# Optimization experiments

Measured on AMD Instinct MI355X. Metric: run time of the kernel, lower is better.

The kernel has to match this reference:

```python
import jax, jax.numpy as jnp
import numpy as np

N, E, IN, K, F, D = 50000, 800000, 256, 4, 64, 2


def setup_inputs() -> dict:
    key = jax.random.key(0)
    ks = jax.random.split(key, 10)
    # CSR rowptr: 0 .. E, nondecreasing, endpoints pinned
    inner = jnp.sort(jax.random.randint(ks[0], (N - 1,), 0, E + 1))
    rowptr = jnp.concatenate([jnp.zeros(1, jnp.int64), inner.astype(jnp.int64), jnp.full(1, E, jnp.int64)])
    colind = jax.random.randint(ks[1], (E,), 0, N).astype(jnp.int64)
    # CSC mirrors (used only by the fused kernel's backward; inert in forward math)
    inner_c = jnp.sort(jax.random.randint(ks[2], (N - 1,), 0, E + 1))
    colptr = jnp.concatenate([jnp.zeros(1, jnp.int64), inner_c.astype(jnp.int64), jnp.full(1, E, jnp.int64)])
    rowind = jax.random.randint(ks[3], (E,), 0, N).astype(jnp.int64)
    permute = jnp.arange(E, dtype=jnp.int64)
    feat = jax.random.normal(ks[4], (N, IN), dtype=jnp.float32)
    pseudo = jax.random.uniform(ks[5], (E, D), dtype=jnp.float32)
    # params: fc weight [K*F, IN] (xavier-normal style scale), mu ~ N(0, 0.1), inv_sigma = 1, bias = 0
    gain = float(np.sqrt(2.0))
    std = gain * float(np.sqrt(2.0 / (IN + K * F)))
    W_fc = jax.random.normal(ks[6], (K * F, IN), dtype=jnp.float32) * std
    mu = jax.random.normal(ks[7], (K, D), dtype=jnp.float32) * 0.1
    inv_sigma = jnp.ones((K, D), dtype=jnp.float32)
    bias = jnp.zeros((F,), dtype=jnp.float32)
    return {"rowptr": rowptr, "colind": colind, "colptr": colptr, "rowind": rowind,
            "permute": permute, "feat": feat, "pseudo": pseudo,
            "W_fc": W_fc, "mu": mu, "inv_sigma": inv_sigma, "bias": bias}


def reference(rowptr, colind, colptr, rowind, permute, feat, pseudo, W_fc, mu, inv_sigma, bias):
    n = feat.shape[0]
    e = colind.shape[0]
    k, d = mu.shape
    f = W_fc.shape[0] // k
    # dense projection: [N, K, F]
    node_feat = (feat @ W_fc.T).reshape(n, k, f)
    # per-edge Gaussian mixture weights: [E, K]
    diff = pseudo[:, None, :] - mu[None, :, :]              # [E, K, D]
    gaussian = jnp.exp(jnp.sum(-0.5 * diff * diff * (inv_sigma[None, :, :] ** 2), axis=-1))
    # multi-head SpMM: gather source feats, weight per kernel, sum kernels (sum commutes
    # with the segment reduction, so fold the head-sum into the edge message): [E, F]
    msg = jnp.einsum('ek,ekf->ef', gaussian, node_feat[colind])
    # destination node of each CSR edge
    dst = jnp.searchsorted(rowptr, jnp.arange(e), side='right') - 1
    rst = jax.ops.segment_sum(msg, dst, num_segments=n)      # [N, F]
    return rst + bias
```

## Files before the change

kernel.cpp:

```cpp
#include <hip/hip_runtime.h>


typedef _Float16 f16;
typedef __attribute__((ext_vector_type(4))) _Float16 f16x4;
typedef __attribute__((ext_vector_type(8))) _Float16 f16x8;
typedef __attribute__((ext_vector_type(4))) float f32x4;

__device__ inline f16x4 cvt4h(float4 v) {
    f16x4 h;
    h.x = (f16)v.x; h.y = (f16)v.y; h.z = (f16)v.z; h.w = (f16)v.w;
    return h;
}

__device__ inline int dot4_i8(int a, int b) {
#if __has_builtin(__builtin_amdgcn_sdot4)
    return __builtin_amdgcn_sdot4(a, b, 0, false);
#else
    return (int)(char)(a)       * (int)(char)(b)
         + (int)(char)(a >> 8)  * (int)(char)(b >> 8)
         + (int)(char)(a >> 16) * (int)(char)(b >> 16)
         + (int)(char)(a >> 24) * (int)(char)(b >> 24);
#endif
}

__global__ __launch_bounds__(256) void convert_W(
    const float* __restrict__ W, f16* __restrict__ Wp)
{
    const int gid = blockIdx.x * 256 + threadIdx.x;
    const int jp = gid >> 6, k4 = gid & 63;
    const int wrow = ((jp >> 4) & 3) * 64 + ((jp >> 6) << 4) + (jp & 15);
    const int k4s = k4 ^ ((jp & 3) << 1);
    reinterpret_cast<f16x4*>(Wp)[jp * 64 + k4s] =
        cvt4h(reinterpret_cast<const float4*>(W)[wrow * 64 + k4]);
}

__global__ __launch_bounds__(256) void gemm_fused(
    const float* __restrict__ feat,
    const f16* __restrict__ Wp,
    char* __restrict__ nfq,
    float* __restrict__ sc,
    int M)
{
    __shared__ char smem[32768 + 16384];
    char* Asb = smem;
    char* Bsb = smem + 32768;
    const int t    = threadIdx.x;
    const int lane = t & 63;
    const int wave = t >> 6;
    const int bm   = blockIdx.x * 64;
    const int l16  = lane & 15;
    const int quad = lane >> 4;
    const int wn   = wave * 64;

    size_t bsrc[4];
#pragma unroll
    for (int j = 0; j < 4; ++j)
        bsrc[j] = (size_t)(wave * 64 + j * 16 + (lane >> 2)) * 256 + (lane & 3) * 8;

    typedef __attribute__((address_space(3))) void lds_t;
    typedef const __attribute__((address_space(1))) void gm_t;

#pragma unroll
    for (int j = 0; j < 4; ++j)
        __builtin_amdgcn_global_load_lds((gm_t*)(Wp + bsrc[j]),
            (lds_t*)(Bsb + (wave * 4 + j) * 1024), 16, 0, 0);

#pragma unroll
    for (int it = 0; it < 8; ++it) {
        const int flat = it * 2048 + t * 8;
        const int row  = flat >> 8;
        const int koff = flat & 255;
        const float* src = feat + (size_t)min(bm + row, M - 1) * 256 + koff;
        const float4 a0 = *reinterpret_cast<const float4*>(src);
        const float4 a1 = *reinterpret_cast<const float4*>(src + 4);
        char* dst = Asb + row * 512 + ((koff * 2) ^ ((row & 7) << 4));
        *reinterpret_cast<f16x4*>(dst)     = cvt4h(a0);
        *reinterpret_cast<f16x4*>(dst + 8) = cvt4h(a1);
    }

    f32x4 acc[4][4];
#pragma unroll
    for (int mi = 0; mi < 4; ++mi)
#pragma unroll
        for (int ni = 0; ni < 4; ++ni)
            acc[mi][ni] = (f32x4){0.f, 0.f, 0.f, 0.f};

    __syncthreads();

    const int axor = (l16 & 7) << 4;
    const int bxor = (l16 & 3) << 4;

#pragma unroll
    for (int ki = 0; ki < 8; ++ki) {
        __builtin_amdgcn_sched_barrier(0);
        asm volatile("s_waitcnt vmcnt(0)" ::: "memory");
        __builtin_amdgcn_sched_barrier(0);

        f16x8 af[4], bfr[4];
#pragma unroll
        for (int mi = 0; mi < 4; ++mi)
            af[mi] = *reinterpret_cast<const f16x8*>(
                Asb + (mi * 16 + l16) * 512 + ((ki * 64 + quad * 16) ^ axor));
#pragma unroll
        for (int ni = 0; ni < 4; ++ni)
            bfr[ni] = *reinterpret_cast<const f16x8*>(
                Bsb + (wn + ni * 16 + l16) * 64 + ((quad << 4) ^ bxor));

        __builtin_amdgcn_sched_barrier(0);
        asm volatile("s_waitcnt lgkmcnt(0)" ::: "memory");
        __builtin_amdgcn_sched_barrier(0);

        if (ki < 7) {
            const int k0 = (ki + 1) * 32;
#pragma unroll
            for (int j = 0; j < 4; ++j)
                __builtin_amdgcn_global_load_lds((gm_t*)(Wp + bsrc[j] + k0),
                    (lds_t*)(Bsb + (wave * 4 + j) * 1024), 16, 0, 0);
        }

#pragma unroll
        for (int mi = 0; mi < 4; ++mi)
#pragma unroll
            for (int ni = 0; ni < 4; ++ni)
                acc[mi][ni] = __builtin_amdgcn_mfma_f32_16x16x32_f16(
                    af[mi], bfr[ni], acc[mi][ni], 0, 0, 0);
    }

#pragma unroll
    for (int mi = 0; mi < 4; ++mi) {
#pragma unroll
        for (int r = 0; r < 4; ++r) {
            float am = 0.f;
#pragma unroll
            for (int ni = 0; ni < 4; ++ni)
                am = fmaxf(am, fabsf(acc[mi][ni][r]));
            am = fmaxf(am, __shfl_xor(am, 1));
            am = fmaxf(am, __shfl_xor(am, 2));
            am = fmaxf(am, __shfl_xor(am, 4));
            am = fmaxf(am, __shfl_xor(am, 8));
            const float sinv = am > 0.f ? 127.f / am : 0.f;
            unsigned pk = 0;
#pragma unroll
            for (int k = 0; k < 4; ++k) {
                const int b = (int)__builtin_rintf(acc[mi][k][r] * sinv);
                pk |= (unsigned)(b & 255) << (8 * k);
            }
            const int rl  = mi * 16 + quad * 4 + r;
            const int row = bm + rl;
            if (row < M) {
                reinterpret_cast<unsigned*>(nfq + (size_t)row * 256)
                    [wave * 16 + l16] = pk;
                if (l16 == 0) sc[row * 4 + wave] = am * (1.f / 16129.f);
            }
        }
    }
}

__global__ __launch_bounds__(256) void edge_aggregate(
    const int* __restrict__ rowptr,
    const int* __restrict__ colind,
    const float* __restrict__ pseudo,
    const char* __restrict__ nfq,
    const float* __restrict__ sc,
    const float* __restrict__ mu,
    const float* __restrict__ inv_sigma,
    const float* __restrict__ bias,
    float* __restrict__ out,
    int N)
{
    const int lane = threadIdx.x & 63;
    const int wid  = blockIdx.x * 4 + (threadIdx.x >> 6);
    const int na   = wid * 2;
    if (na >= N) return;
    const int nb   = na + 1;
    const bool hb  = nb < N;

    const int fo   = lane & 15;
    const int eg   = lane >> 4;
    const int qoff = fo << 4;
    const int goff = fo >> 2;

    const int kk = lane >> 4;
    const float mx = mu[2 * kk], my = mu[2 * kk + 1];
    const float sa = inv_sigma[2 * kk], sb = inv_sigma[2 * kk + 1];
    const float C  = -0.5f * 1.4426950408889634f;
    const float cx = C * sa * sa, cy = C * sb * sb;
    const int   sh = kk * 8;

    auto gpack = [&](int ec, int e0, int e1) -> int {
        const int exm = ec + fo;
        const bool gv = exm < e1;
        const int safe = (e1 > e0) ? (e1 - 1) : 0;
        const int ex  = gv ? exm : safe;
        const float2 p = *reinterpret_cast<const float2*>(pseudo + 2 * (size_t)ex);
        const float dx = p.x - mx, dy = p.y - my;
        const float g = exp2f(fmaf(dy * dy, cy, dx * dx * cx));
        int b = gv ? (((int)(g * 127.f + 0.5f)) << sh) : 0;
        b |= __shfl_xor(b, 16);
        b |= __shfl_xor(b, 32);
        return b;
    };

    const int ea0 = rowptr[na];
    const int ea1 = rowptr[na + 1];
    const int eb0 = ea1;
    const int eb1 = hb ? rowptr[nb + 1] : ea1;

    const int safea = (ea1 > ea0) ? (ea1 - 1) : 0;
    int cfo_a = colind[min(ea0 + fo, safea)];
    int cfo_b = 0, gpk_b = 0;
    if (hb) {
        const int safeb = (eb1 > eb0) ? (eb1 - 1) : 0;
        cfo_b = colind[min(eb0 + fo, safeb)];
        gpk_b = gpack(eb0, eb0, eb1);
    }
    int gpk_a = gpack(ea0, ea0, ea1);

    float a0 = 0.f, a1 = 0.f, a2 = 0.f, a3 = 0.f;
    {
        int gpk = gpk_a, cfo = cfo_a;
        for (int ec = ea0; ec < ea1; ec += 16) {
            int4  q[4];
            float s[4];
            int   gq[4];
#pragma unroll
            for (int gi = 0; gi < 4; ++gi) {
                const int c = __shfl(cfo, gi * 4 + eg);
                q[gi]  = *reinterpret_cast<const int4*>(
                             nfq + ((size_t)c << 8) + qoff);
                s[gi]  = sc[c * 4 + goff];
                gq[gi] = __shfl(gpk, gi * 4 + eg);
            }
            const int ecn = ec + 16;
            int gpk_n = 0, cfo_n = cfo;
            if (ecn < ea1) {
                cfo_n = colind[min(ecn + fo, ea1 - 1)];
                gpk_n = gpack(ecn, ea0, ea1);
            }
#pragma unroll
            for (int gi = 0; gi < 4; ++gi) {
                a0 = fmaf(s[gi], (float)dot4_i8(q[gi].x, gq[gi]), a0);
                a1 = fmaf(s[gi], (float)dot4_i8(q[gi].y, gq[gi]), a1);
                a2 = fmaf(s[gi], (float)dot4_i8(q[gi].z, gq[gi]), a2);
                a3 = fmaf(s[gi], (float)dot4_i8(q[gi].w, gq[gi]), a3);
            }
            gpk = gpk_n; cfo = cfo_n;
        }
    }
    a0 += __shfl_xor(a0, 16); a0 += __shfl_xor(a0, 32);
    a1 += __shfl_xor(a1, 16); a1 += __shfl_xor(a1, 32);
    a2 += __shfl_xor(a2, 16); a2 += __shfl_xor(a2, 32);
    a3 += __shfl_xor(a3, 16); a3 += __shfl_xor(a3, 32);
    if (lane < 16) {
        const float4 b4 = reinterpret_cast<const float4*>(bias)[fo];
        float4 o;
        o.x = a0 + b4.x; o.y = a1 + b4.y; o.z = a2 + b4.z; o.w = a3 + b4.w;
        reinterpret_cast<float4*>(out + ((size_t)na << 6))[fo] = o;
    }

    if (!hb) return;
    float b0 = 0.f, b1 = 0.f, b2 = 0.f, b3 = 0.f;
    {
        int gpk = gpk_b, cfo = cfo_b;
        for (int ec = eb0; ec < eb1; ec += 16) {
            int4  q[4];
            float s[4];
            int   gq[4];
#pragma unroll
            for (int gi = 0; gi < 4; ++gi) {
                const int c = __shfl(cfo, gi * 4 + eg);
                q[gi]  = *reinterpret_cast<const int4*>(
                             nfq + ((size_t)c << 8) + qoff);
                s[gi]  = sc[c * 4 + goff];
                gq[gi] = __shfl(gpk, gi * 4 + eg);
            }
            const int ecn = ec + 16;
            int gpk_n = 0, cfo_n = cfo;
            if (ecn < eb1) {
                cfo_n = colind[min(ecn + fo, eb1 - 1)];
                gpk_n = gpack(ecn, eb0, eb1);
            }
#pragma unroll
            for (int gi = 0; gi < 4; ++gi) {
                b0 = fmaf(s[gi], (float)dot4_i8(q[gi].x, gq[gi]), b0);
                b1 = fmaf(s[gi], (float)dot4_i8(q[gi].y, gq[gi]), b1);
                b2 = fmaf(s[gi], (float)dot4_i8(q[gi].z, gq[gi]), b2);
                b3 = fmaf(s[gi], (float)dot4_i8(q[gi].w, gq[gi]), b3);
            }
            gpk = gpk_n; cfo = cfo_n;
        }
    }
    b0 += __shfl_xor(b0, 16); b0 += __shfl_xor(b0, 32);
    b1 += __shfl_xor(b1, 16); b1 += __shfl_xor(b1, 32);
    b2 += __shfl_xor(b2, 16); b2 += __shfl_xor(b2, 32);
    b3 += __shfl_xor(b3, 16); b3 += __shfl_xor(b3, 32);
    if (lane < 16) {
        const float4 b4 = reinterpret_cast<const float4*>(bias)[fo];
        float4 o;
        o.x = b0 + b4.x; o.y = b1 + b4.y; o.z = b2 + b4.z; o.w = b3 + b4.w;
        reinterpret_cast<float4*>(out + ((size_t)nb << 6))[fo] = o;
    }
}

extern "C" void kernel_launch(void* const* d_in, const int* in_sizes, int n_in,
                              void* d_out, int out_size, void* d_ws, size_t ws_size,
                              hipStream_t stream)
{
    const int*   rowptr    = (const int*)d_in[0];
    const int*   colind    = (const int*)d_in[1];
    const float* feat      = (const float*)d_in[5];
    const float* pseudo    = (const float*)d_in[6];
    const float* W_fc      = (const float*)d_in[7];
    const float* mu        = (const float*)d_in[8];
    const float* inv_sigma = (const float*)d_in[9];
    const float* bias      = (const float*)d_in[10];
    float* out = (float*)d_out;

    const int N = in_sizes[0] - 1;
    char*  nfq = (char*)d_ws;
    float* sc  = (float*)(nfq + (size_t)N * 256);
    f16*   Wp  = (f16*)d_out;

    hipLaunchKernelGGL(convert_W, dim3(64), dim3(256), 0, stream, W_fc, Wp);

    hipLaunchKernelGGL(gemm_fused, dim3((N + 63) / 64), dim3(256), 0, stream,
                       feat, Wp, nfq, sc, N);

    hipLaunchKernelGGL(edge_aggregate, dim3((N + 7) / 8), dim3(256), 0, stream,
                       rowptr, colind, pseudo, nfq, sc, mu, inv_sigma, bias, out, N);
}
```

Measured before the change: 162.5 us.

## Load GEMM operands directly from global memory, dropping LDS staging

Removes the shared-memory staging of the fp32 feature tile and the swizzled f16 weight tile in the projection GEMM. Each lane now reads its MFMA fragments straight from global memory, converting features to f16 in registers, and the weight pre-conversion no longer swizzles. Dropping LDS and block barriers allows a higher occupancy hint (3 blocks per CU). The cost is that every wave reloads the same A rows and B columns from global or L2, with less coalesced 32-byte strided accesses and no cross-wave reuse.

```diff
diff --git a/kernel.cpp b/kernel.cpp
--- a/kernel.cpp
+++ b/kernel.cpp
@@ -29,21 +29,17 @@
     const int gid = blockIdx.x * 256 + threadIdx.x;
     const int jp = gid >> 6, k4 = gid & 63;
     const int wrow = ((jp >> 4) & 3) * 64 + ((jp >> 6) << 4) + (jp & 15);
-    const int k4s = k4 ^ ((jp & 3) << 1);
-    reinterpret_cast<f16x4*>(Wp)[jp * 64 + k4s] =
+    reinterpret_cast<f16x4*>(Wp)[jp * 64 + k4] =
         cvt4h(reinterpret_cast<const float4*>(W)[wrow * 64 + k4]);
 }
 
-__global__ __launch_bounds__(256) void gemm_fused(
+__global__ __launch_bounds__(256, 3) void gemm_fused(
     const float* __restrict__ feat,
     const f16* __restrict__ Wp,
     char* __restrict__ nfq,
     float* __restrict__ sc,
     int M)
 {
-    __shared__ char smem[32768 + 16384];
-    char* Asb = smem;
-    char* Bsb = smem + 32768;
     const int t    = threadIdx.x;
     const int lane = t & 63;
     const int wave = t >> 6;
@@ -52,31 +48,14 @@
     const int quad = lane >> 4;
     const int wn   = wave * 64;
 
-    size_t bsrc[4];
-#pragma unroll
-    for (int j = 0; j < 4; ++j)
-        bsrc[j] = (size_t)(wave * 64 + j * 16 + (lane >> 2)) * 256 + (lane & 3) * 8;
-
-    typedef __attribute__((address_space(3))) void lds_t;
-    typedef const __attribute__((address_space(1))) void gm_t;
-
-#pragma unroll
-    for (int j = 0; j < 4; ++j)
-        __builtin_amdgcn_global_load_lds((gm_t*)(Wp + bsrc[j]),
-            (lds_t*)(Bsb + (wave * 4 + j) * 1024), 16, 0, 0);
-
-#pragma unroll
-    for (int it = 0; it < 8; ++it) {
-        const int flat = it * 2048 + t * 8;
-        const int row  = flat >> 8;
-        const int koff = flat & 255;
-        const float* src = feat + (size_t)min(bm + row, M - 1) * 256 + koff;
-        const float4 a0 = *reinterpret_cast<const float4*>(src);
-        const float4 a1 = *reinterpret_cast<const float4*>(src + 4);
-        char* dst = Asb + row * 512 + ((koff * 2) ^ ((row & 7) << 4));
-        *reinterpret_cast<f16x4*>(dst)     = cvt4h(a0);
-        *reinterpret_cast<f16x4*>(dst + 8) = cvt4h(a1);
-    }
+    const float* arow[4];
+#pragma unroll
+    for (int mi = 0; mi < 4; ++mi)
+        arow[mi] = feat + (size_t)min(bm + mi * 16 + l16, M - 1) * 256;
+    const f16* brow[4];
+#pragma unroll
+    for (int ni = 0; ni < 4; ++ni)
+        brow[ni] = Wp + (size_t)(wn + ni * 16 + l16) * 256;
 
     f32x4 acc[4][4];
 #pragma unroll
@@ -85,45 +64,27 @@
         for (int ni = 0; ni < 4; ++ni)
             acc[mi][ni] = (f32x4){0.f, 0.f, 0.f, 0.f};
 
-    __syncthreads();
-
-    const int axor = (l16 & 7) << 4;
-    const int bxor = (l16 & 3) << 4;
-
 #pragma unroll
     for (int ki = 0; ki < 8; ++ki) {
-        __builtin_amdgcn_sched_barrier(0);
-        asm volatile("s_waitcnt vmcnt(0)" ::: "memory");
-        __builtin_amdgcn_sched_barrier(0);
-
-        f16x8 af[4], bfr[4];
-#pragma unroll
-        for (int mi = 0; mi < 4; ++mi)
-            af[mi] = *reinterpret_cast<const f16x8*>(
-                Asb + (mi * 16 + l16) * 512 + ((ki * 64 + quad * 16) ^ axor));
+        const int ko = ki * 32 + quad * 8;
+        f16x8 af[4], bf[4];
 #pragma unroll
         for (int ni = 0; ni < 4; ++ni)
-            bfr[ni] = *reinterpret_cast<const f16x8*>(
-                Bsb + (wn + ni * 16 + l16) * 64 + ((quad << 4) ^ bxor));
-
-        __builtin_amdgcn_sched_barrier(0);
-        asm volatile("s_waitcnt lgkmcnt(0)" ::: "memory");
-        __builtin_amdgcn_sched_barrier(0);
-
-        if (ki < 7) {
-            const int k0 = (ki + 1) * 32;
-#pragma unroll
-            for (int j = 0; j < 4; ++j)
-                __builtin_amdgcn_global_load_lds((gm_t*)(Wp + bsrc[j] + k0),
-                    (lds_t*)(Bsb + (wave * 4 + j) * 1024), 16, 0, 0);
-        }
-
+            bf[ni] = *reinterpret_cast<const f16x8*>(brow[ni] + ko);
+#pragma unroll
+        for (int mi = 0; mi < 4; ++mi) {
+            const float4 a0 = *reinterpret_cast<const float4*>(arow[mi] + ko);
+            const float4 a1 = *reinterpret_cast<const float4*>(arow[mi] + ko + 4);
+            const f16x4 h0 = cvt4h(a0);
+            const f16x4 h1 = cvt4h(a1);
+            af[mi] = (f16x8){h0.x, h0.y, h0.z, h0.w, h1.x, h1.y, h1.z, h1.w};
+        }
 #pragma unroll
         for (int mi = 0; mi < 4; ++mi)
 #pragma unroll
             for (int ni = 0; ni < 4; ++ni)
                 acc[mi][ni] = __builtin_amdgcn_mfma_f32_16x16x32_f16(
-                    af[mi], bfr[ni], acc[mi][ni], 0, 0, 0);
+                    af[mi], bf[ni], acc[mi][ni], 0, 0, 0);
     }
 
 #pragma unroll
```

Result: slower. 190.3 us (+17.1%).
